# Optimization experiments

Hardware: AMD Instinct MI355X
Metric: run time of the kernel (lower is better)

Reference implementation:

```python
import jax, jax.numpy as jnp
import numpy as np

B, LQ, LKV, D, DV = 8, 2048, 2048, 128, 128


def setup_inputs() -> dict:
    key = jax.random.key(0)
    kq, kk, kv = jax.random.split(key, 3)
    return {
        "query": jax.random.normal(kq, (B, LQ, D), dtype=jnp.float32),
        "key": jax.random.normal(kk, (B, LKV, D), dtype=jnp.float32),
        "value": jax.random.normal(kv, (B, LKV, DV), dtype=jnp.float32),
    }


def reference(query, key, value):
    # score_fn: scaled dot-product  score = Q K^T / sqrt(Dq)
    scale = 1.0 / jnp.sqrt(jnp.asarray(query.shape[-1], query.dtype))
    score = jnp.einsum("bqd,bkd->bqk", query, key) * scale  # (B, Lq, Lkv)
    attention_weights = jax.nn.softmax(score, axis=-1)
    context_vector = jnp.einsum("bqk,bkv->bqv", attention_weights, value)
    return attention_weights, context_vector
```

## Files before the change

kernel.cpp:

```cpp
#include <hip/hip_runtime.h>

#define BB    8
#define LQN   2048
#define LKVN  2048
#define DQ    128
#define DVN   128
#define QT    32
#define KTI   128
#define NT    (LKVN / KTI)
#define OSTR  132

typedef short short8 __attribute__((ext_vector_type(8)));
typedef float f32x4  __attribute__((ext_vector_type(4)));
typedef int   int4v  __attribute__((ext_vector_type(4)));

__device__ __forceinline__ short f2bf(float f) {
  unsigned u = __builtin_bit_cast(unsigned, f);
  u += 0x7fffu + ((u >> 16) & 1u);
  return (short)(u >> 16);
}

__device__ __forceinline__ int packbf(float a, float b) {
  unsigned lo = (unsigned short)f2bf(a);
  unsigned hi = (unsigned short)f2bf(b);
  return (int)(lo | (hi << 16));
}

__global__ __launch_bounds__(256) void pre_kernel(const float* __restrict__ K,
                                                  const float* __restrict__ V,
                                                  short* __restrict__ Kb,
                                                  short* __restrict__ Vt) {
  __shared__ float tile[128][33];
  if (blockIdx.x >= 512) {
    int i = (blockIdx.x - 512) * 256 + threadIdx.x;
    size_t off = (size_t)i * 8;
    float4 a = *(const float4*)(K + off);
    float4 c = *(const float4*)(K + off + 4);
    short8 o;
    o[0] = f2bf(a.x); o[1] = f2bf(a.y); o[2] = f2bf(a.z); o[3] = f2bf(a.w);
    o[4] = f2bf(c.x); o[5] = f2bf(c.y); o[6] = f2bf(c.z); o[7] = f2bf(c.w);
    *(short8*)(Kb + off) = o;
    return;
  }
  const int bx  = blockIdx.x;
  const int kv0 = (bx & 15) * 128;
  const int dv0 = ((bx >> 4) & 3) * 32;
  const int b   = bx >> 6;
  const int tid = threadIdx.x;
  const float* src = V + ((size_t)b * LKVN + kv0) * DVN + dv0;
#pragma unroll
  for (int it = 0; it < 4; ++it) {
    int idx = it * 256 + tid;
    int r = idx >> 3, c4 = idx & 7;
    float4 v = *(const float4*)(src + (size_t)r * DVN + c4 * 4);
    tile[r][c4 * 4 + 0] = v.x;
    tile[r][c4 * 4 + 1] = v.y;
    tile[r][c4 * 4 + 2] = v.z;
    tile[r][c4 * 4 + 3] = v.w;
  }
  __syncthreads();
  short* dst = Vt + ((size_t)b * DVN + dv0) * LKVN + kv0;
#pragma unroll
  for (int it = 0; it < 2; ++it) {
    int idx = it * 256 + tid;
    int row = idx >> 4, ch = idx & 15;
    short8 o;
#pragma unroll
    for (int j = 0; j < 8; ++j) o[j] = f2bf(tile[ch * 8 + j][row]);
    *(short8*)(dst + (size_t)row * LKVN + ch * 8) = o;
  }
}

__global__ __launch_bounds__(512, 4) void attn_kernel(const float* __restrict__ Q,
                                                      const short* __restrict__ Kb,
                                                      const short* __restrict__ Vt,
                                                      float* __restrict__ W,
                                                      float* __restrict__ O) {
  __shared__ __align__(16) char smem[33792];
  __shared__ float red_l[4][QT];
  short* k_lds = (short*)smem;
  float (*osum)[QT][OSTR] = (float (*)[QT][OSTR])smem;

  const int tid  = threadIdx.x;
  const int w    = tid >> 6;
  const int lane = tid & 63;
  const int n    = lane & 15;
  const int qd   = lane >> 4;
  const int s    = w & 3;
  const int g    = w >> 2;
  const int b    = blockIdx.x & 7;
  const int q0   = (blockIdx.x >> 3) * QT;

  const short* Kbase = Kb + (size_t)b * LKVN * DQ;
  const short* Vw = Vt + ((size_t)b * DVN + n) * LKVN + s * 32 + qd * 8;
  float* Wrow = W + ((size_t)b * LQN + q0 + g * 16 + n) * LKVN + s * 32 + qd * 4;

  const int sr = tid >> 4;
  const int sc = tid & 15;
  const int swz_w = (sc * 8) ^ ((sr & 7) << 3);

  const int krow = s * 32 + n;
  const int rswz = (n & 7) << 3;

  short8 qf[4];
  {
    const float* Qrow = Q + ((size_t)b * LQN + q0 + g * 16 + n) * DQ + qd * 8;
#pragma unroll
    for (int ks = 0; ks < 4; ++ks) {
      float4 f0 = *(const float4*)(Qrow + ks * 32);
      float4 f1 = *(const float4*)(Qrow + ks * 32 + 4);
      short8 o;
      o[0] = f2bf(f0.x); o[1] = f2bf(f0.y); o[2] = f2bf(f0.z); o[3] = f2bf(f0.w);
      o[4] = f2bf(f1.x); o[5] = f2bf(f1.y); o[6] = f2bf(f1.z); o[7] = f2bf(f1.w);
      qf[ks] = o;
    }
  }

  const float scale = 0.08838834764831845f;
  float l_part = 0.f;
  short8 kreg[4];

#pragma unroll
  for (int j = 0; j < 4; ++j)
    kreg[j] = *(const short8*)(Kbase + (size_t)(j * 32 + sr) * DQ + sc * 8);
#pragma unroll
  for (int j = 0; j < 4; ++j)
    *(short8*)&k_lds[(j * 32 + sr) * 128 + swz_w] = kreg[j];

  for (int t = 0; t < NT; ++t) {
    __syncthreads();
    if (t + 1 < NT) {
      const short* src = Kbase + (size_t)(t + 1) * KTI * DQ;
#pragma unroll
      for (int j = 0; j < 4; ++j)
        kreg[j] = *(const short8*)(src + (size_t)(j * 32 + sr) * DQ + sc * 8);
    }
#pragma unroll
    for (int t2 = 0; t2 < 2; ++t2) {
      f32x4 acc = {0.f, 0.f, 0.f, 0.f};
#pragma unroll
      for (int ks = 0; ks < 4; ++ks) {
        short8 kf = *(const short8*)&k_lds[(krow + t2 * 16) * 128 +
                                           ((ks * 32 + qd * 8) ^ rswz)];
        acc = __builtin_amdgcn_mfma_f32_16x16x32_bf16(kf, qf[ks], acc, 0, 0, 0);
      }
#pragma unroll
      for (int r = 0; r < 4; ++r) l_part += __expf(acc[r] * scale);
    }
    __syncthreads();
    if (t + 1 < NT) {
#pragma unroll
      for (int j = 0; j < 4; ++j)
        *(short8*)&k_lds[(j * 32 + sr) * 128 + swz_w] = kreg[j];
    }
  }

  l_part += __shfl_xor(l_part, 16, 64);
  l_part += __shfl_xor(l_part, 32, 64);
  if (lane < 16) red_l[s][g * 16 + lane] = l_part;
  __syncthreads();
  const float rinv =
      1.0f / (red_l[0][g * 16 + n] + red_l[1][g * 16 + n] +
              red_l[2][g * 16 + n] + red_l[3][g * 16 + n]);

  const int srcA = n + ((qd & 1) << 5);
  const int srcB = srcA + 16;
  const int sel  = qd >> 1;

  f32x4 oacc[8];
#pragma unroll
  for (int dvg = 0; dvg < 8; ++dvg) oacc[dvg] = (f32x4){0.f, 0.f, 0.f, 0.f};

#pragma unroll
  for (int j = 0; j < 4; ++j)
    kreg[j] = *(const short8*)(Kbase + (size_t)(j * 32 + sr) * DQ + sc * 8);
#pragma unroll
  for (int j = 0; j < 4; ++j)
    *(short8*)&k_lds[(j * 32 + sr) * 128 + swz_w] = kreg[j];

  for (int t = 0; t < NT; ++t) {
    __syncthreads();
    f32x4 acc[2];
    __builtin_amdgcn_s_setprio(1);
#pragma unroll
    for (int t2 = 0; t2 < 2; ++t2) {
      acc[t2] = (f32x4){0.f, 0.f, 0.f, 0.f};
#pragma unroll
      for (int ks = 0; ks < 4; ++ks) {
        short8 kf = *(const short8*)&k_lds[(krow + t2 * 16) * 128 +
                                           ((ks * 32 + qd * 8) ^ rswz)];
        acc[t2] = __builtin_amdgcn_mfma_f32_16x16x32_bf16(kf, qf[ks], acc[t2], 0, 0, 0);
      }
    }
    __builtin_amdgcn_s_setprio(0);

    if (t + 1 < NT) {
      const short* src = Kbase + (size_t)(t + 1) * KTI * DQ;
#pragma unroll
      for (int j = 0; j < 4; ++j)
        kreg[j] = *(const short8*)(src + (size_t)(j * 32 + sr) * DQ + sc * 8);
    }
    short8 vf[8];
#pragma unroll
    for (int dvg = 0; dvg < 8; ++dvg)
      vf[dvg] = *(const short8*)(Vw + (size_t)(dvg * 16) * LKVN + t * KTI);

    int pk[2][2];
#pragma unroll
    for (int t2 = 0; t2 < 2; ++t2) {
      float p0 = __expf(acc[t2][0] * scale) * rinv;
      float p1 = __expf(acc[t2][1] * scale) * rinv;
      float p2 = __expf(acc[t2][2] * scale) * rinv;
      float p3 = __expf(acc[t2][3] * scale) * rinv;
      f32x4 st = {p0, p1, p2, p3};
      *(f32x4*)(Wrow + t * KTI + t2 * 16) = st;
      pk[t2][0] = packbf(p0, p1);
      pk[t2][1] = packbf(p2, p3);
    }
    int a0 = __shfl(pk[0][0], srcA, 64);
    int b0 = __shfl(pk[1][0], srcA, 64);
    int a1 = __shfl(pk[0][1], srcA, 64);
    int b1 = __shfl(pk[1][1], srcA, 64);
    int a2 = __shfl(pk[0][0], srcB, 64);
    int b2 = __shfl(pk[1][0], srcB, 64);
    int a3 = __shfl(pk[0][1], srcB, 64);
    int b3 = __shfl(pk[1][1], srcB, 64);
    int4v bi;
    bi[0] = sel ? b0 : a0;
    bi[1] = sel ? b1 : a1;
    bi[2] = sel ? b2 : a2;
    bi[3] = sel ? b3 : a3;
    short8 bfr = __builtin_bit_cast(short8, bi);

    __builtin_amdgcn_s_setprio(1);
#pragma unroll
    for (int dvg = 0; dvg < 8; ++dvg)
      oacc[dvg] = __builtin_amdgcn_mfma_f32_16x16x32_bf16(vf[dvg], bfr, oacc[dvg], 0, 0, 0);
    __builtin_amdgcn_s_setprio(0);

    __syncthreads();
    if (t + 1 < NT) {
#pragma unroll
      for (int j = 0; j < 4; ++j)
        *(short8*)&k_lds[(j * 32 + sr) * 128 + swz_w] = kreg[j];
    }
  }

  if (s < 2) {
#pragma unroll
    for (int dvg = 0; dvg < 8; ++dvg)
      *(f32x4*)&osum[s][g * 16 + n][dvg * 16 + qd * 4] = oacc[dvg];
  }
  __syncthreads();
  if (s >= 2) {
#pragma unroll
    for (int dvg = 0; dvg < 8; ++dvg) {
      f32x4* p = (f32x4*)&osum[s - 2][g * 16 + n][dvg * 16 + qd * 4];
      *p = *p + oacc[dvg];
    }
  }
  __syncthreads();

  float* Ob = O + ((size_t)b * LQN + q0) * DVN;
  const int qq = tid >> 4;
  const int c0 = (tid & 15) * 8;
#pragma unroll
  for (int c = 0; c < 2; ++c) {
    f32x4 s0 = *(const f32x4*)&osum[0][qq][c0 + c * 4];
    f32x4 s1 = *(const f32x4*)&osum[1][qq][c0 + c * 4];
    s0 = s0 + s1;
    *(f32x4*)(Ob + (size_t)qq * DVN + c0 + c * 4) = s0;
  }
}

extern "C" void kernel_launch(void* const* d_in, const int* in_sizes, int n_in,
                              void* d_out, int out_size, void* d_ws, size_t ws_size,
                              hipStream_t stream) {
  const float* Q = (const float*)d_in[0];
  const float* K = (const float*)d_in[1];
  const float* V = (const float*)d_in[2];
  float* W = (float*)d_out;
  float* O = W + (size_t)BB * LQN * LKVN;
  short* Kb = (short*)d_ws;
  short* Vt = Kb + (size_t)BB * LKVN * DQ;

  pre_kernel<<<1536, 256, 0, stream>>>(K, V, Kb, Vt);
  attn_kernel<<<512, 512, 0, stream>>>(Q, Kb, Vt, W, O);
}
```

Measured before the change: 236.5 us.

## Double-buffer K tiles in LDS via direct global-to-LDS loads

Replaces the register-staged K tile copy (global load into registers, then an LDS store after a barrier) with global_load_lds DMA into a double-buffered LDS region. The next tile is issued into the alternate buffer while the current one is consumed, which removes one barrier per iteration and frees the kreg registers. The cost is twice the LDS footprint (64KB), which may reduce occupancy from the requested 4 blocks per CU. It also relies on the XOR swizzle being reproduced correctly through the per-lane global source addresses.

```diff
diff --git a/kernel.cpp b/kernel.cpp
--- a/kernel.cpp
+++ b/kernel.cpp
@@ -24,6 +24,12 @@
   unsigned lo = (unsigned short)f2bf(a);
   unsigned hi = (unsigned short)f2bf(b);
   return (int)(lo | (hi << 16));
+}
+
+__device__ __forceinline__ void gld_lds16(const void* g, void* l) {
+  __builtin_amdgcn_global_load_lds(
+      (const __attribute__((address_space(1))) unsigned int*)g,
+      (__attribute__((address_space(3))) unsigned int*)l, 16, 0, 0);
 }
 
 __global__ __launch_bounds__(256) void pre_kernel(const float* __restrict__ K,
@@ -76,10 +82,9 @@
                                                       const short* __restrict__ Vt,
                                                       float* __restrict__ W,
                                                       float* __restrict__ O) {
-  __shared__ __align__(16) char smem[33792];
+  __shared__ __align__(16) short k_lds[2 * 16384];
   __shared__ float red_l[4][QT];
-  short* k_lds = (short*)smem;
-  float (*osum)[QT][OSTR] = (float (*)[QT][OSTR])smem;
+  float (*osum)[QT][OSTR] = (float (*)[QT][OSTR])k_lds;
 
   const int tid  = threadIdx.x;
   const int w    = tid >> 6;
@@ -95,11 +100,25 @@
   const short* Vw = Vt + ((size_t)b * DVN + n) * LKVN + s * 32 + qd * 8;
   float* Wrow = W + ((size_t)b * LQN + q0 + g * 16 + n) * LKVN + s * 32 + qd * 4;
 
-  const int sr = tid >> 4;
-  const int sc = tid & 15;
-  const int swz_w = (sc * 8) ^ ((sr & 7) << 3);
-
-  const int krow = s * 32 + n;
+  const int drow = lane >> 4;
+  const short* KdmaE = Kbase + (size_t)(16 * w + drow) * DQ +
+                       (((lane & 15) ^ drow) * 8);
+  const short* KdmaO = Kbase + (size_t)(16 * w + drow) * DQ +
+                       (((lane & 15) ^ (4 + drow)) * 8);
+  short* ldsw = k_lds + (w * 4) * 512;
+
+#define STAGE(bsel, t)                                                          \
+  {                                                                             \
+    const short* ge = KdmaE + (size_t)(t) * KTI * DQ;                           \
+    const short* go = KdmaO + (size_t)(t) * KTI * DQ;                           \
+    short* lb = ldsw + (bsel) * 16384;                                          \
+    gld_lds16(ge,           lb);                                                \
+    gld_lds16(go + 4 * DQ,  lb + 512);                                          \
+    gld_lds16(ge + 8 * DQ,  lb + 1024);                                         \
+    gld_lds16(go + 12 * DQ, lb + 1536);                                         \
+  }
+
+  const int krow = (s * 32 + n) * 128;
   const int rswz = (n & 7) << 3;
 
   short8 qf[4];
@@ -118,46 +137,32 @@
 
   const float scale = 0.08838834764831845f;
   float l_part = 0.f;
-  short8 kreg[4];
-
-#pragma unroll
-  for (int j = 0; j < 4; ++j)
-    kreg[j] = *(const short8*)(Kbase + (size_t)(j * 32 + sr) * DQ + sc * 8);
-#pragma unroll
-  for (int j = 0; j < 4; ++j)
-    *(short8*)&k_lds[(j * 32 + sr) * 128 + swz_w] = kreg[j];
-
+
+  STAGE(0, 0)
+  __syncthreads();
+  int cur = 0;
   for (int t = 0; t < NT; ++t) {
-    __syncthreads();
-    if (t + 1 < NT) {
-      const short* src = Kbase + (size_t)(t + 1) * KTI * DQ;
-#pragma unroll
-      for (int j = 0; j < 4; ++j)
-        kreg[j] = *(const short8*)(src + (size_t)(j * 32 + sr) * DQ + sc * 8);
-    }
+    if (t + 1 < NT) STAGE(cur ^ 1, t + 1)
+    const short* kb = k_lds + cur * 16384;
 #pragma unroll
     for (int t2 = 0; t2 < 2; ++t2) {
       f32x4 acc = {0.f, 0.f, 0.f, 0.f};
 #pragma unroll
       for (int ks = 0; ks < 4; ++ks) {
-        short8 kf = *(const short8*)&k_lds[(krow + t2 * 16) * 128 +
-                                           ((ks * 32 + qd * 8) ^ rswz)];
+        short8 kf = *(const short8*)&kb[krow + t2 * 2048 + ((ks * 32 + qd * 8) ^ rswz)];
         acc = __builtin_amdgcn_mfma_f32_16x16x32_bf16(kf, qf[ks], acc, 0, 0, 0);
       }
 #pragma unroll
       for (int r = 0; r < 4; ++r) l_part += __expf(acc[r] * scale);
     }
     __syncthreads();
-    if (t + 1 < NT) {
-#pragma unroll
-      for (int j = 0; j < 4; ++j)
-        *(short8*)&k_lds[(j * 32 + sr) * 128 + swz_w] = kreg[j];
-    }
+    cur ^= 1;
   }
 
   l_part += __shfl_xor(l_part, 16, 64);
   l_part += __shfl_xor(l_part, 32, 64);
   if (lane < 16) red_l[s][g * 16 + lane] = l_part;
+  STAGE(0, 0)
   __syncthreads();
   const float rinv =
       1.0f / (red_l[0][g * 16 + n] + red_l[1][g * 16 + n] +
@@ -171,15 +176,10 @@
 #pragma unroll
   for (int dvg = 0; dvg < 8; ++dvg) oacc[dvg] = (f32x4){0.f, 0.f, 0.f, 0.f};
 
-#pragma unroll
-  for (int j = 0; j < 4; ++j)
-    kreg[j] = *(const short8*)(Kbase + (size_t)(j * 32 + sr) * DQ + sc * 8);
-#pragma unroll
-  for (int j = 0; j < 4; ++j)
-    *(short8*)&k_lds[(j * 32 + sr) * 128 + swz_w] = kreg[j];
-
+  cur = 0;
   for (int t = 0; t < NT; ++t) {
-    __syncthreads();
+    if (t + 1 < NT) STAGE(cur ^ 1, t + 1)
+    const short* kb = k_lds + cur * 16384;
     f32x4 acc[2];
     __builtin_amdgcn_s_setprio(1);
 #pragma unroll
@@ -187,19 +187,12 @@
       acc[t2] = (f32x4){0.f, 0.f, 0.f, 0.f};
 #pragma unroll
       for (int ks = 0; ks < 4; ++ks) {
-        short8 kf = *(const short8*)&k_lds[(krow + t2 * 16) * 128 +
-                                           ((ks * 32 + qd * 8) ^ rswz)];
+        short8 kf = *(const short8*)&kb[krow + t2 * 2048 + ((ks * 32 + qd * 8) ^ rswz)];
         acc[t2] = __builtin_amdgcn_mfma_f32_16x16x32_bf16(kf, qf[ks], acc[t2], 0, 0, 0);
       }
     }
     __builtin_amdgcn_s_setprio(0);
 
-    if (t + 1 < NT) {
-      const short* src = Kbase + (size_t)(t + 1) * KTI * DQ;
-#pragma unroll
-      for (int j = 0; j < 4; ++j)
-        kreg[j] = *(const short8*)(src + (size_t)(j * 32 + sr) * DQ + sc * 8);
-    }
     short8 vf[8];
 #pragma unroll
     for (int dvg = 0; dvg < 8; ++dvg)
@@ -239,11 +232,7 @@
     __builtin_amdgcn_s_setprio(0);
 
     __syncthreads();
-    if (t + 1 < NT) {
-#pragma unroll
-      for (int j = 0; j < 4; ++j)
-        *(short8*)&k_lds[(j * 32 + sr) * 128 + swz_w] = kreg[j];
-    }
+    cur ^= 1;
   }
 
   if (s < 2) {
```

Result: no change. 232.5 us (-1.7%).
